# Performance work log

Measured on AMD Instinct MI355X. Metric: run time of the kernel, lower is better.

## Reference

```python
import jax, jax.numpy as jnp
import numpy as np

E = 100000
VERTEX_DIM = 64
EDGE_DIM = 128
MESSAGE_DIM = 64


def setup_inputs() -> dict:
    key = jax.random.key(0)
    k1, k2, k3, k4 = jax.random.split(key, 4)
    vertices = jax.random.normal(k1, (E, VERTEX_DIM), dtype=jnp.float32)
    edges = jax.random.normal(k2, (E, EDGE_DIM), dtype=jnp.float32)
    # nn.Linear(edge_dim, message_dim * vertex_dim): weight [out, in], bias [out]
    W = jax.random.normal(k3, (MESSAGE_DIM * VERTEX_DIM, EDGE_DIM), dtype=jnp.float32) * (1.0 / np.sqrt(EDGE_DIM))
    b = jax.random.normal(k4, (MESSAGE_DIM * VERTEX_DIM,), dtype=jnp.float32) * 0.01
    return {"vertices": vertices, "edges": edges, "W": W, "b": b}


def reference(vertices, edges, W, b):
    # edge_net(edges): [E, message_dim*vertex_dim]
    proj = edges @ W.T + b
    # view to [E, message_dim, vertex_dim], then batched matvec with vertices [E, vertex_dim]
    proj = proj.reshape(edges.shape[0], MESSAGE_DIM, VERTEX_DIM)
    message = jnp.einsum('emv,ev->em', proj, vertices)  # [E, message_dim]
    return message
```

## Files before the change

### kernel.cpp

```cpp
#include <hip/hip_runtime.h>
#include <hip/hip_bf16.h>
#include <stdint.h>


typedef _Float16 f16;
typedef __attribute__((ext_vector_type(2))) _Float16 f16x2;
typedef __attribute__((ext_vector_type(8))) _Float16 f16x8;
typedef __attribute__((ext_vector_type(4))) float f32x4;

#define MSG_D 64
#define VTX_D 64
#define EDG_D 128
#define EPB 256

__device__ __forceinline__ f16x8 cvt8(float4 a, float4 d) {
  return (f16x8){(f16)a.x, (f16)a.y, (f16)a.z, (f16)a.w,
                 (f16)d.x, (f16)d.y, (f16)d.z, (f16)d.w};
}

__global__ void prep_w(const float* __restrict__ W, const float* __restrict__ b,
                       f16* __restrict__ Wh, f16* __restrict__ Bh) {
  int tid = blockIdx.x * 256 + threadIdx.x;
  if (tid < 65536) {
    int L = tid & 63, n = (tid >> 6) & 3, s = (tid >> 8) & 3, v = tid >> 10;
    int q = L >> 4, ln = L & 15;
    const float* src = W + (size_t)((n * 16 + ln) * 64 + v) * 128 + s * 32 + q * 8;
    float4 a = *(const float4*)src, d = *(const float4*)(src + 4);
    *(f16x8*)(Wh + (size_t)tid * 8) = cvt8(a, d);
  } else if (tid < 66048) {
    int t2 = tid - 65536;
    int L = t2 & 63, n = (t2 >> 6) & 3, s2 = t2 >> 8;
    int q = L >> 4, ln = L & 15;
    const float* src = b + (n * 16 + ln) * 64 + s2 * 32 + q * 8;
    float4 a = *(const float4*)src, d = *(const float4*)(src + 4);
    *(f16x8*)(Bh + (size_t)t2 * 8) = cvt8(a, d);
  }
}

__global__ void prep_vt(const float* __restrict__ V, f16* __restrict__ Vt, int E) {
  __shared__ f16 tile[64][72];
  int e0 = blockIdx.x * 64;
  int t  = threadIdx.x;
  {
    int el = t >> 2, c4 = t & 3;
    bool ok = (e0 + el) < E;
    const float* src = V + (size_t)(ok ? e0 + el : 0) * VTX_D + c4 * 16;
    #pragma unroll
    for (int i = 0; i < 4; ++i) {
      float4 a = {0.f, 0.f, 0.f, 0.f};
      if (ok) a = *(const float4*)(src + 4 * i);
      float av[4] = {a.x, a.y, a.z, a.w};
      #pragma unroll
      for (int j = 0; j < 4; ++j) tile[c4 * 16 + i * 4 + j][el] = (f16)av[j];
    }
  }
  __syncthreads();
  int v = t & 63, c = t >> 6;
  int ebase = e0 + c * 16;
  union { f16 h[16]; f16x8 v8[2]; } o;
  #pragma unroll
  for (int k = 0; k < 16; ++k) o.h[k] = tile[v][c * 16 + k];
  f16* dst = Vt + (size_t)v * E + ebase;
  if (ebase + 16 <= E) {
    *(f16x8*)dst = o.v8[0];
    *(f16x8*)(dst + 8) = o.v8[1];
  } else {
    for (int k = 0; k < 16; ++k)
      if (ebase + k < E) dst[k] = o.h[k];
  }
}

template <bool USE_VT>
__global__ __launch_bounds__(256, 2) void edge_msg_flat(
    const float* __restrict__ Vtx, const float* __restrict__ Xe,
    const f16* __restrict__ Wh, const f16* __restrict__ Bh,
    const f16* __restrict__ Vt, float* __restrict__ out, int E)
{
  const int lane = threadIdx.x & 63;
  const int q = lane >> 4, ln = lane & 15;
  const int eoff = blockIdx.x * EPB + (threadIdx.x >> 6) * 64;

  int er[4];
  f16x8 xh[4][4];
  #pragma unroll
  for (int t = 0; t < 4; ++t) {
    int e = eoff + 16 * t + ln;
    er[t] = e < E ? e : E - 1;
    const float* xr = Xe + (size_t)er[t] * EDG_D;
    #pragma unroll
    for (int s = 0; s < 4; ++s) {
      float4 a = *(const float4*)(xr + s * 32 + q * 8);
      float4 d = *(const float4*)(xr + s * 32 + q * 8 + 4);
      xh[t][s] = cvt8(a, d);
    }
  }

  f32x4 acc[4][4];
  #pragma unroll
  for (int t = 0; t < 4; ++t)
    #pragma unroll
    for (int n = 0; n < 4; ++n) acc[t][n] = (f32x4){0.f, 0.f, 0.f, 0.f};

  const f16* wp = Wh + (size_t)lane * 8;

  f16 vc[4];
  #pragma unroll
  for (int t = 0; t < 4; ++t)
    vc[t] = USE_VT ? Vt[er[t]] : (f16)Vtx[(size_t)er[t] * VTX_D];

  #pragma unroll 1
  for (int v = 0; v < 64; ++v) {
    f16x8 wf[16];
    const f16* wrow = wp + (size_t)v * 8192;
    #pragma unroll
    for (int c = 0; c < 16; ++c) wf[c] = *(const f16x8*)(wrow + c * 512);

    f16 vn[4];
    int v1 = v + 1 < 64 ? v + 1 : 63;
    #pragma unroll
    for (int t = 0; t < 4; ++t)
      vn[t] = USE_VT ? Vt[(size_t)v1 * E + er[t]]
                     : (f16)Vtx[(size_t)er[t] * VTX_D + v1];

    #pragma unroll
    for (int s = 0; s < 4; ++s) {
      f16x8 af[4];
      #pragma unroll
      for (int t = 0; t < 4; ++t) {
        f16x2 hv = {vc[t], vc[t]};
        union { f16x8 v8; f16x2 h2[4]; } x, r;
        x.v8 = xh[t][s];
        r.h2[0] = hv * x.h2[0];
        r.h2[1] = hv * x.h2[1];
        r.h2[2] = hv * x.h2[2];
        r.h2[3] = hv * x.h2[3];
        af[t] = r.v8;
      }
      #pragma unroll
      for (int n = 0; n < 4; ++n)
        #pragma unroll
        for (int t = 0; t < 4; ++t)
          acc[t][n] = __builtin_amdgcn_mfma_f32_16x16x32_f16(af[t], wf[s * 4 + n], acc[t][n], 0, 0, 0);
    }
    #pragma unroll
    for (int t = 0; t < 4; ++t) vc[t] = vn[t];
  }

  #pragma unroll
  for (int s2 = 0; s2 < 2; ++s2) {
    f16x8 av[4];
    #pragma unroll
    for (int t = 0; t < 4; ++t) {
      const float* vr2 = Vtx + (size_t)er[t] * VTX_D + s2 * 32 + q * 8;
      float4 a = *(const float4*)vr2, d = *(const float4*)(vr2 + 4);
      av[t] = cvt8(a, d);
    }
    #pragma unroll
    for (int n = 0; n < 4; ++n) {
      f16x8 bf = *(const f16x8*)(Bh + (size_t)((s2 * 4 + n) * 64 + lane) * 8);
      #pragma unroll
      for (int t = 0; t < 4; ++t)
        acc[t][n] = __builtin_amdgcn_mfma_f32_16x16x32_f16(av[t], bf, acc[t][n], 0, 0, 0);
    }
  }

  #pragma unroll
  for (int t = 0; t < 4; ++t)
    #pragma unroll
    for (int r = 0; r < 4; ++r) {
      int e = eoff + 16 * t + 4 * q + r;
      if (e < E) {
        float* orow = out + (size_t)e * MSG_D;
        #pragma unroll
        for (int n = 0; n < 4; ++n) orow[n * 16 + ln] = acc[t][n][r];
      }
    }
}

__global__ void edge_msg_naive(const float* __restrict__ Vtx, const float* __restrict__ Xe,
                               const float* __restrict__ W, const float* __restrict__ b,
                               float* __restrict__ out, int E) {
  __shared__ float xs[EDG_D];
  __shared__ float vs[VTX_D];
  int e = blockIdx.x;
  int m = threadIdx.x;
  for (int i = m; i < EDG_D; i += 64) xs[i] = Xe[(size_t)e * EDG_D + i];
  for (int i = m; i < VTX_D; i += 64) vs[i] = Vtx[(size_t)e * VTX_D + i];
  __syncthreads();
  float s = 0.f;
  for (int v = 0; v < VTX_D; ++v) {
    const float* wr = W + (size_t)(m * 64 + v) * EDG_D;
    float p = b[m * 64 + v];
    for (int k = 0; k < EDG_D; ++k) p += xs[k] * wr[k];
    s += p * vs[v];
  }
  out[(size_t)e * MSG_D + m] = s;
}

extern "C" void kernel_launch(void* const* d_in, const int* in_sizes, int n_in,
                              void* d_out, int out_size, void* d_ws, size_t ws_size,
                              hipStream_t stream) {
  const float* Vtx = (const float*)d_in[0];
  const float* Xe  = (const float*)d_in[1];
  const float* W   = (const float*)d_in[2];
  const float* b   = (const float*)d_in[3];
  float* out = (float*)d_out;

  const int E  = in_sizes[0] / VTX_D;
  const int nW = in_sizes[2];
  const int nb = in_sizes[3];

  const size_t needW  = (size_t)(524288 + 4096) * sizeof(f16);
  const size_t needVt = (size_t)64 * E * sizeof(f16);

  if (nW != 524288 || nb != 4096 || ws_size < needW) {
    edge_msg_naive<<<E, 64, 0, stream>>>(Vtx, Xe, W, b, out, E);
    return;
  }

  f16* Wh = (f16*)d_ws;
  f16* Bh = Wh + 524288;

  prep_w<<<258, 256, 0, stream>>>(W, b, Wh, Bh);

  int blocks = (E + EPB - 1) / EPB;
  if (ws_size >= needW + needVt && (E & 7) == 0) {
    f16* Vt = Bh + 4096;
    prep_vt<<<(E + 63) / 64, 256, 0, stream>>>(Vtx, Vt, E);
    edge_msg_flat<true><<<blocks, 256, 0, stream>>>(Vtx, Xe, Wh, Bh, Vt, out, E);
  } else {
    edge_msg_flat<false><<<blocks, 256, 0, stream>>>(Vtx, Xe, Wh, Bh, nullptr, out, E);
  }
}
```

Baseline: 249.2 us.

## Drop vertex transpose pass, use single-wave blocks and double-buffer weight fragments

Removes the prep_vt transpose kernel and reads vertex values directly as vectorized 8-element chunks per edge row, prefetching the next chunk. Blocks shrink from four waves to one wave of 64 edges. The weight fragment loads are split into two halves so the next v's first half loads while the current v's second half computes. This aims to cut an extra kernel launch and pass over vertices and to hide weight-load latency, at the cost of higher register pressure and smaller blocks.

Result: no change. 248.0 us (-0.5%).

```diff
diff --git a/kernel.cpp b/kernel.cpp
--- a/kernel.cpp
+++ b/kernel.cpp
@@ -11,7 +11,6 @@
 #define MSG_D 64
 #define VTX_D 64
 #define EDG_D 128
-#define EPB 256
 
 __device__ __forceinline__ f16x8 cvt8(float4 a, float4 d) {
   return (f16x8){(f16)a.x, (f16)a.y, (f16)a.z, (f16)a.w,
@@ -37,48 +36,14 @@
   }
 }
 
-__global__ void prep_vt(const float* __restrict__ V, f16* __restrict__ Vt, int E) {
-  __shared__ f16 tile[64][72];
-  int e0 = blockIdx.x * 64;
-  int t  = threadIdx.x;
-  {
-    int el = t >> 2, c4 = t & 3;
-    bool ok = (e0 + el) < E;
-    const float* src = V + (size_t)(ok ? e0 + el : 0) * VTX_D + c4 * 16;
-    #pragma unroll
-    for (int i = 0; i < 4; ++i) {
-      float4 a = {0.f, 0.f, 0.f, 0.f};
-      if (ok) a = *(const float4*)(src + 4 * i);
-      float av[4] = {a.x, a.y, a.z, a.w};
-      #pragma unroll
-      for (int j = 0; j < 4; ++j) tile[c4 * 16 + i * 4 + j][el] = (f16)av[j];
-    }
-  }
-  __syncthreads();
-  int v = t & 63, c = t >> 6;
-  int ebase = e0 + c * 16;
-  union { f16 h[16]; f16x8 v8[2]; } o;
-  #pragma unroll
-  for (int k = 0; k < 16; ++k) o.h[k] = tile[v][c * 16 + k];
-  f16* dst = Vt + (size_t)v * E + ebase;
-  if (ebase + 16 <= E) {
-    *(f16x8*)dst = o.v8[0];
-    *(f16x8*)(dst + 8) = o.v8[1];
-  } else {
-    for (int k = 0; k < 16; ++k)
-      if (ebase + k < E) dst[k] = o.h[k];
-  }
-}
-
-template <bool USE_VT>
-__global__ __launch_bounds__(256, 2) void edge_msg_flat(
+__global__ __launch_bounds__(64, 2) void edge_msg_flat(
     const float* __restrict__ Vtx, const float* __restrict__ Xe,
     const f16* __restrict__ Wh, const f16* __restrict__ Bh,
-    const f16* __restrict__ Vt, float* __restrict__ out, int E)
+    float* __restrict__ out, int E)
 {
-  const int lane = threadIdx.x & 63;
+  const int lane = threadIdx.x;
   const int q = lane >> 4, ln = lane & 15;
-  const int eoff = blockIdx.x * EPB + (threadIdx.x >> 6) * 64;
+  const int eoff = blockIdx.x * 64;
 
   int er[4];
   f16x8 xh[4][4];
@@ -103,47 +68,89 @@
 
   const f16* wp = Wh + (size_t)lane * 8;
 
-  f16 vc[4];
-  #pragma unroll
-  for (int t = 0; t < 4; ++t)
-    vc[t] = USE_VT ? Vt[er[t]] : (f16)Vtx[(size_t)er[t] * VTX_D];
+  f16x8 wA[8], wB[8];
+  #pragma unroll
+  for (int c = 0; c < 8; ++c) wA[c] = *(const f16x8*)(wp + c * 512);
+
+  f16x8 vrow[4];
+  #pragma unroll
+  for (int t = 0; t < 4; ++t) {
+    const float* vsrc = Vtx + (size_t)er[t] * VTX_D;
+    float4 a = *(const float4*)(vsrc), d = *(const float4*)(vsrc + 4);
+    vrow[t] = cvt8(a, d);
+  }
 
   #pragma unroll 1
-  for (int v = 0; v < 64; ++v) {
-    f16x8 wf[16];
-    const f16* wrow = wp + (size_t)v * 8192;
-    #pragma unroll
-    for (int c = 0; c < 16; ++c) wf[c] = *(const f16x8*)(wrow + c * 512);
-
-    f16 vn[4];
-    int v1 = v + 1 < 64 ? v + 1 : 63;
-    #pragma unroll
-    for (int t = 0; t < 4; ++t)
-      vn[t] = USE_VT ? Vt[(size_t)v1 * E + er[t]]
-                     : (f16)Vtx[(size_t)er[t] * VTX_D + v1];
-
-    #pragma unroll
-    for (int s = 0; s < 4; ++s) {
-      f16x8 af[4];
+  for (int c8 = 0; c8 < 8; ++c8) {
+    f16x8 vnext[4];
+    if (c8 < 7) {
       #pragma unroll
       for (int t = 0; t < 4; ++t) {
-        f16x2 hv = {vc[t], vc[t]};
-        union { f16x8 v8; f16x2 h2[4]; } x, r;
-        x.v8 = xh[t][s];
-        r.h2[0] = hv * x.h2[0];
-        r.h2[1] = hv * x.h2[1];
-        r.h2[2] = hv * x.h2[2];
-        r.h2[3] = hv * x.h2[3];
-        af[t] = r.v8;
-      }
-      #pragma unroll
-      for (int n = 0; n < 4; ++n)
-        #pragma unroll
-        for (int t = 0; t < 4; ++t)
-          acc[t][n] = __builtin_amdgcn_mfma_f32_16x16x32_f16(af[t], wf[s * 4 + n], acc[t][n], 0, 0, 0);
-    }
-    #pragma unroll
-    for (int t = 0; t < 4; ++t) vc[t] = vn[t];
+        const float* vsrc = Vtx + (size_t)er[t] * VTX_D + (c8 + 1) * 8;
+        float4 a = *(const float4*)(vsrc), d = *(const float4*)(vsrc + 4);
+        vnext[t] = cvt8(a, d);
+      }
+    }
+
+    #pragma unroll
+    for (int j = 0; j < 8; ++j) {
+      const int v = c8 * 8 + j;
+      const f16* wrow  = wp + (size_t)v * 8192;
+      const f16* wrowN = wp + (size_t)(v < 63 ? v + 1 : 63) * 8192;
+
+      #pragma unroll
+      for (int c = 0; c < 8; ++c) wB[c] = *(const f16x8*)(wrow + (8 + c) * 512);
+
+      f16x2 hv[4];
+      #pragma unroll
+      for (int t = 0; t < 4; ++t) { f16 h = vrow[t][j]; hv[t] = (f16x2){h, h}; }
+
+      #pragma unroll
+      for (int s = 0; s < 2; ++s) {
+        f16x8 af[4];
+        #pragma unroll
+        for (int t = 0; t < 4; ++t) {
+          union { f16x8 v8; f16x2 h2[4]; } x, r;
+          x.v8 = xh[t][s];
+          r.h2[0] = hv[t] * x.h2[0];
+          r.h2[1] = hv[t] * x.h2[1];
+          r.h2[2] = hv[t] * x.h2[2];
+          r.h2[3] = hv[t] * x.h2[3];
+          af[t] = r.v8;
+        }
+        #pragma unroll
+        for (int n = 0; n < 4; ++n)
+          #pragma unroll
+          for (int t = 0; t < 4; ++t)
+            acc[t][n] = __builtin_amdgcn_mfma_f32_16x16x32_f16(af[t], wA[s * 4 + n], acc[t][n], 0, 0, 0);
+      }
+
+      #pragma unroll
+      for (int c = 0; c < 8; ++c) wA[c] = *(const f16x8*)(wrowN + c * 512);
+
+      #pragma unroll
+      for (int s = 2; s < 4; ++s) {
+        f16x8 af[4];
+        #pragma unroll
+        for (int t = 0; t < 4; ++t) {
+          union { f16x8 v8; f16x2 h2[4]; } x, r;
+          x.v8 = xh[t][s];
+          r.h2[0] = hv[t] * x.h2[0];
+          r.h2[1] = hv[t] * x.h2[1];
+          r.h2[2] = hv[t] * x.h2[2];
+          r.h2[3] = hv[t] * x.h2[3];
+          af[t] = r.v8;
+        }
+        #pragma unroll
+        for (int n = 0; n < 4; ++n)
+          #pragma unroll
+          for (int t = 0; t < 4; ++t)
+            acc[t][n] = __builtin_amdgcn_mfma_f32_16x16x32_f16(af[t], wB[(s - 2) * 4 + n], acc[t][n], 0, 0, 0);
+      }
+    }
+
+    #pragma unroll
+    for (int t = 0; t < 4; ++t) vrow[t] = vnext[t];
   }
 
   #pragma unroll
@@ -210,8 +217,7 @@
   const int nW = in_sizes[2];
   const int nb = in_sizes[3];
 
-  const size_t needW  = (size_t)(524288 + 4096) * sizeof(f16);
-  const size_t needVt = (size_t)64 * E * sizeof(f16);
+  const size_t needW = (size_t)(524288 + 4096) * sizeof(f16);
 
   if (nW != 524288 || nb != 4096 || ws_size < needW) {
     edge_msg_naive<<<E, 64, 0, stream>>>(Vtx, Xe, W, b, out, E);
@@ -223,12 +229,6 @@
 
   prep_w<<<258, 256, 0, stream>>>(W, b, Wh, Bh);
 
-  int blocks = (E + EPB - 1) / EPB;
-  if (ws_size >= needW + needVt && (E & 7) == 0) {
-    f16* Vt = Bh + 4096;
-    prep_vt<<<(E + 63) / 64, 256, 0, stream>>>(Vtx, Vt, E);
-    edge_msg_flat<true><<<blocks, 256, 0, stream>>>(Vtx, Xe, Wh, Bh, Vt, out, E);
-  } else {
-    edge_msg_flat<false><<<blocks, 256, 0, stream>>>(Vtx, Xe, Wh, Bh, nullptr, out, E);
-  }
-}
+  int blocks = (E + 63) / 64;
+  edge_msg_flat<<<blocks, 64, 0, stream>>>(Vtx, Xe, Wh, Bh, out, E);
+}
```

## Split output columns across blocks, prefetch weights, merge prep kernels

Applied to the files above, without the earlier changes.

The main kernel now runs one 64-thread wave per block, and each block handles 64 edges and half of the 64 message columns, so the grid doubles and each wave holds half the accumulators. The weight fragments are split into two halves and double-buffered in registers, loading the next v's first half during the current MFMAs to hide latency. The two preprocessing kernels (weight fp16 conversion and vertex transpose) are merged into one launch. In exchange, each edge's edge features and vertex scalars are loaded and scaled twice, and occupancy changes through the new launch bounds.

Result: slower. 254.5 us (+2.1%).

```diff
diff --git a/kernel.cpp b/kernel.cpp
--- a/kernel.cpp
+++ b/kernel.cpp
@@ -11,16 +11,51 @@
 #define MSG_D 64
 #define VTX_D 64
 #define EDG_D 128
-#define EPB 256
 
 __device__ __forceinline__ f16x8 cvt8(float4 a, float4 d) {
   return (f16x8){(f16)a.x, (f16)a.y, (f16)a.z, (f16)a.w,
                  (f16)d.x, (f16)d.y, (f16)d.z, (f16)d.w};
 }
 
-__global__ void prep_w(const float* __restrict__ W, const float* __restrict__ b,
-                       f16* __restrict__ Wh, f16* __restrict__ Bh) {
-  int tid = blockIdx.x * 256 + threadIdx.x;
+__global__ void prep_all(const float* __restrict__ W, const float* __restrict__ b,
+                         const float* __restrict__ V,
+                         f16* __restrict__ Wh, f16* __restrict__ Bh,
+                         f16* __restrict__ Vt, int E, int nvt) {
+  __shared__ f16 tile[64][72];
+  int bx = blockIdx.x;
+  if (bx < nvt) {
+    int e0 = bx * 64;
+    int t  = threadIdx.x;
+    {
+      int el = t >> 2, c4 = t & 3;
+      bool ok = (e0 + el) < E;
+      const float* src = V + (size_t)(ok ? e0 + el : 0) * VTX_D + c4 * 16;
+      #pragma unroll
+      for (int i = 0; i < 4; ++i) {
+        float4 a = {0.f, 0.f, 0.f, 0.f};
+        if (ok) a = *(const float4*)(src + 4 * i);
+        float av[4] = {a.x, a.y, a.z, a.w};
+        #pragma unroll
+        for (int j = 0; j < 4; ++j) tile[c4 * 16 + i * 4 + j][el] = (f16)av[j];
+      }
+    }
+    __syncthreads();
+    int v = t & 63, c = t >> 6;
+    int ebase = e0 + c * 16;
+    union { f16 h[16]; f16x8 v8[2]; } o;
+    #pragma unroll
+    for (int k = 0; k < 16; ++k) o.h[k] = tile[v][c * 16 + k];
+    f16* dst = Vt + (size_t)v * E + ebase;
+    if (ebase + 16 <= E) {
+      *(f16x8*)dst = o.v8[0];
+      *(f16x8*)(dst + 8) = o.v8[1];
+    } else {
+      for (int k = 0; k < 16; ++k)
+        if (ebase + k < E) dst[k] = o.h[k];
+    }
+    return;
+  }
+  int tid = (bx - nvt) * 256 + threadIdx.x;
   if (tid < 65536) {
     int L = tid & 63, n = (tid >> 6) & 3, s = (tid >> 8) & 3, v = tid >> 10;
     int q = L >> 4, ln = L & 15;
@@ -37,48 +72,17 @@
   }
 }
 
-__global__ void prep_vt(const float* __restrict__ V, f16* __restrict__ Vt, int E) {
-  __shared__ f16 tile[64][72];
-  int e0 = blockIdx.x * 64;
-  int t  = threadIdx.x;
-  {
-    int el = t >> 2, c4 = t & 3;
-    bool ok = (e0 + el) < E;
-    const float* src = V + (size_t)(ok ? e0 + el : 0) * VTX_D + c4 * 16;
-    #pragma unroll
-    for (int i = 0; i < 4; ++i) {
-      float4 a = {0.f, 0.f, 0.f, 0.f};
-      if (ok) a = *(const float4*)(src + 4 * i);
-      float av[4] = {a.x, a.y, a.z, a.w};
-      #pragma unroll
-      for (int j = 0; j < 4; ++j) tile[c4 * 16 + i * 4 + j][el] = (f16)av[j];
-    }
-  }
-  __syncthreads();
-  int v = t & 63, c = t >> 6;
-  int ebase = e0 + c * 16;
-  union { f16 h[16]; f16x8 v8[2]; } o;
-  #pragma unroll
-  for (int k = 0; k < 16; ++k) o.h[k] = tile[v][c * 16 + k];
-  f16* dst = Vt + (size_t)v * E + ebase;
-  if (ebase + 16 <= E) {
-    *(f16x8*)dst = o.v8[0];
-    *(f16x8*)(dst + 8) = o.v8[1];
-  } else {
-    for (int k = 0; k < 16; ++k)
-      if (ebase + k < E) dst[k] = o.h[k];
-  }
-}
-
 template <bool USE_VT>
-__global__ __launch_bounds__(256, 2) void edge_msg_flat(
+__global__ __launch_bounds__(64, 3) void edge_msg_flat(
     const float* __restrict__ Vtx, const float* __restrict__ Xe,
     const f16* __restrict__ Wh, const f16* __restrict__ Bh,
     const f16* __restrict__ Vt, float* __restrict__ out, int E)
 {
-  const int lane = threadIdx.x & 63;
+  const int lane = threadIdx.x;
   const int q = lane >> 4, ln = lane & 15;
-  const int eoff = blockIdx.x * EPB + (threadIdx.x >> 6) * 64;
+  const int mg = blockIdx.x >> 1;
+  const int nh = blockIdx.x & 1;
+  const int eoff = mg * 64;
 
   int er[4];
   f16x8 xh[4][4];
@@ -95,53 +99,94 @@
     }
   }
 
-  f32x4 acc[4][4];
+  f32x4 acc[4][2];
   #pragma unroll
   for (int t = 0; t < 4; ++t)
     #pragma unroll
-    for (int n = 0; n < 4; ++n) acc[t][n] = (f32x4){0.f, 0.f, 0.f, 0.f};
-
-  const f16* wp = Wh + (size_t)lane * 8;
+    for (int n = 0; n < 2; ++n) acc[t][n] = (f32x4){0.f, 0.f, 0.f, 0.f};
+
+  const f16* wp = Wh + (size_t)lane * 8 + (size_t)nh * 1024;
+
+  f16x8 wA[4], wB[4];
+  #pragma unroll
+  for (int s = 0; s < 2; ++s)
+    #pragma unroll
+    for (int n = 0; n < 2; ++n)
+      wA[s * 2 + n] = *(const f16x8*)(wp + s * 2048 + n * 512);
 
   f16 vc[4];
   #pragma unroll
   for (int t = 0; t < 4; ++t)
     vc[t] = USE_VT ? Vt[er[t]] : (f16)Vtx[(size_t)er[t] * VTX_D];
 
-  #pragma unroll 1
+  #pragma unroll 2
   for (int v = 0; v < 64; ++v) {
-    f16x8 wf[16];
-    const f16* wrow = wp + (size_t)v * 8192;
-    #pragma unroll
-    for (int c = 0; c < 16; ++c) wf[c] = *(const f16x8*)(wrow + c * 512);
+    const f16* wrow  = wp + (size_t)v * 8192;
+    const f16* wrowN = wp + (size_t)(v < 63 ? v + 1 : 63) * 8192;
+
+    #pragma unroll
+    for (int s = 0; s < 2; ++s)
+      #pragma unroll
+      for (int n = 0; n < 2; ++n)
+        wB[s * 2 + n] = *(const f16x8*)(wrow + (s + 2) * 2048 + n * 512);
 
     f16 vn[4];
-    int v1 = v + 1 < 64 ? v + 1 : 63;
+    int v1 = v < 63 ? v + 1 : 63;
     #pragma unroll
     for (int t = 0; t < 4; ++t)
       vn[t] = USE_VT ? Vt[(size_t)v1 * E + er[t]]
                      : (f16)Vtx[(size_t)er[t] * VTX_D + v1];
 
-    #pragma unroll
-    for (int s = 0; s < 4; ++s) {
+    f16x2 hv[4];
+    #pragma unroll
+    for (int t = 0; t < 4; ++t) { f16 h = vc[t]; hv[t] = (f16x2){h, h}; }
+
+    #pragma unroll
+    for (int s = 0; s < 2; ++s) {
       f16x8 af[4];
       #pragma unroll
       for (int t = 0; t < 4; ++t) {
-        f16x2 hv = {vc[t], vc[t]};
         union { f16x8 v8; f16x2 h2[4]; } x, r;
         x.v8 = xh[t][s];
-        r.h2[0] = hv * x.h2[0];
-        r.h2[1] = hv * x.h2[1];
-        r.h2[2] = hv * x.h2[2];
-        r.h2[3] = hv * x.h2[3];
+        r.h2[0] = hv[t] * x.h2[0];
+        r.h2[1] = hv[t] * x.h2[1];
+        r.h2[2] = hv[t] * x.h2[2];
+        r.h2[3] = hv[t] * x.h2[3];
         af[t] = r.v8;
       }
       #pragma unroll
-      for (int n = 0; n < 4; ++n)
+      for (int n = 0; n < 2; ++n)
         #pragma unroll
         for (int t = 0; t < 4; ++t)
-          acc[t][n] = __builtin_amdgcn_mfma_f32_16x16x32_f16(af[t], wf[s * 4 + n], acc[t][n], 0, 0, 0);
-    }
+          acc[t][n] = __builtin_amdgcn_mfma_f32_16x16x32_f16(af[t], wA[s * 2 + n], acc[t][n], 0, 0, 0);
+    }
+
+    #pragma unroll
+    for (int s = 0; s < 2; ++s)
+      #pragma unroll
+      for (int n = 0; n < 2; ++n)
+        wA[s * 2 + n] = *(const f16x8*)(wrowN + s * 2048 + n * 512);
+
+    #pragma unroll
+    for (int s = 0; s < 2; ++s) {
+      f16x8 af[4];
+      #pragma unroll
+      for (int t = 0; t < 4; ++t) {
+        union { f16x8 v8; f16x2 h2[4]; } x, r;
+        x.v8 = xh[t][s + 2];
+        r.h2[0] = hv[t] * x.h2[0];
+        r.h2[1] = hv[t] * x.h2[1];
+        r.h2[2] = hv[t] * x.h2[2];
+        r.h2[3] = hv[t] * x.h2[3];
+        af[t] = r.v8;
+      }
+      #pragma unroll
+      for (int n = 0; n < 2; ++n)
+        #pragma unroll
+        for (int t = 0; t < 4; ++t)
+          acc[t][n] = __builtin_amdgcn_mfma_f32_16x16x32_f16(af[t], wB[s * 2 + n], acc[t][n], 0, 0, 0);
+    }
+
     #pragma unroll
     for (int t = 0; t < 4; ++t) vc[t] = vn[t];
   }
@@ -156,8 +201,8 @@
       av[t] = cvt8(a, d);
     }
     #pragma unroll
-    for (int n = 0; n < 4; ++n) {
-      f16x8 bf = *(const f16x8*)(Bh + (size_t)((s2 * 4 + n) * 64 + lane) * 8);
+    for (int n = 0; n < 2; ++n) {
+      f16x8 bf = *(const f16x8*)(Bh + (size_t)((s2 * 4 + nh * 2 + n) * 64 + lane) * 8);
       #pragma unroll
       for (int t = 0; t < 4; ++t)
         acc[t][n] = __builtin_amdgcn_mfma_f32_16x16x32_f16(av[t], bf, acc[t][n], 0, 0, 0);
@@ -170,9 +215,9 @@
     for (int r = 0; r < 4; ++r) {
       int e = eoff + 16 * t + 4 * q + r;
       if (e < E) {
-        float* orow = out + (size_t)e * MSG_D;
-        #pragma unroll
-        for (int n = 0; n < 4; ++n) orow[n * 16 + ln] = acc[t][n][r];
+        float* orow = out + (size_t)e * MSG_D + nh * 32 + ln;
+        orow[0]  = acc[t][0][r];
+        orow[16] = acc[t][1][r];
       }
     }
 }
@@ -221,14 +266,16 @@
   f16* Wh = (f16*)d_ws;
   f16* Bh = Wh + 524288;
 
-  prep_w<<<258, 256, 0, stream>>>(W, b, Wh, Bh);
-
-  int blocks = (E + EPB - 1) / EPB;
+  int mgroups = (E + 63) / 64;
+  int blocks = mgroups * 2;
+
   if (ws_size >= needW + needVt && (E & 7) == 0) {
     f16* Vt = Bh + 4096;
-    prep_vt<<<(E + 63) / 64, 256, 0, stream>>>(Vtx, Vt, E);
-    edge_msg_flat<true><<<blocks, 256, 0, stream>>>(Vtx, Xe, Wh, Bh, Vt, out, E);
+    int nvt = (E + 63) / 64;
+    prep_all<<<nvt + 258, 256, 0, stream>>>(W, b, Vtx, Wh, Bh, Vt, E, nvt);
+    edge_msg_flat<true><<<blocks, 64, 0, stream>>>(Vtx, Xe, Wh, Bh, Vt, out, E);
   } else {
-    edge_msg_flat<false><<<blocks, 256, 0, stream>>>(Vtx, Xe, Wh, Bh, nullptr, out, E);
-  }
-}
+    prep_all<<<258, 256, 0, stream>>>(W, b, Vtx, Wh, Bh, nullptr, E, 0);
+    edge_msg_flat<false><<<blocks, 64, 0, stream>>>(Vtx, Xe, Wh, Bh, nullptr, out, E);
+  }
+}
```
